# Performance work log

Measured on AMD Instinct MI355X. Metric: run time of the kernel, lower is better.

## Reference

```python
import jax, jax.numpy as jnp
import numpy as np

B, D = 32, 512
N_IMG, N_KN = 50000, 8192
C = 32          # num_classes
R = 16          # image_retrieval_number
K = 8           # knowledge_retrieval_number
NEG = -1e9


def setup_inputs() -> dict:
    key = jax.random.key(0)
    k1, k2, k3, k4, k5 = jax.random.split(key, 5)
    return {
        'query_embeddings': jax.random.normal(k1, (B, D), dtype=jnp.float32),
        'all_image_embeddings': jax.random.normal(k2, (N_IMG, D), dtype=jnp.float32),
        'all_knowledge_embeddings': jax.random.normal(k3, (N_KN, D), dtype=jnp.float32),
        'image_labels': jax.random.randint(k4, (N_IMG,), 0, C, dtype=jnp.int32),
        'knowledge_labels': jax.random.randint(k5, (N_KN,), 0, C, dtype=jnp.int32),
    }


def reference(query_embeddings, all_image_embeddings, all_knowledge_embeddings,
              image_labels, knowledge_labels):
    classes = jnp.arange(C, dtype=jnp.int32)
    img_class_mask = image_labels[None, :] == classes[:, None]       # [C, N_img]
    kn_class_mask = knowledge_labels[None, :] == classes[:, None]    # [C, N_kn]

    # per-class masked similarity retrieval of images
    sims = query_embeddings @ all_image_embeddings.T                 # [B, N_img]
    masked = jnp.where(img_class_mask[None], sims[:, None, :], NEG)  # [B, C, N_img]
    img_vals, img_idx = jax.lax.top_k(masked, R)                     # [B, C, R]
    img_w = jax.nn.softmax(img_vals, axis=-1)
    similar_images = all_image_embeddings[img_idx]                   # [B, C, R, D]

    # image fusion (average of query and attention-weighted retrieved context)
    fused_img = jnp.einsum('bcr,bcrd->bcd', img_w, similar_images)
    enhanced_images = 0.5 * (query_embeddings[:, None, :] + fused_img)  # [B, C, D]

    # class-masked knowledge retrieval for every retrieved image
    ksims = jnp.einsum('bcrd,nd->bcrn', similar_images, all_knowledge_embeddings)
    kmasked = jnp.where(kn_class_mask[None, :, None, :], ksims, NEG)  # [B, C, R, N_kn]
    k_vals, k_idx = jax.lax.top_k(kmasked, K)                         # [B, C, R, K]
    k_w = jax.nn.softmax(k_vals, axis=-1)
    selected_knowledge = all_knowledge_embeddings[k_idx]              # [B, C, R, K, D]

    # knowledge fusion: weight over K, then over R with image weights, average w/ query
    fused_k = jnp.einsum('bcrk,bcrkd->bcrd', k_w, selected_knowledge)
    fused_k = jnp.einsum('bcr,bcrd->bcd', img_w, fused_k)
    enhanced_knowledge = 0.5 * (query_embeddings[:, None, :] + fused_k)  # [B, C, D]

    return enhanced_images, enhanced_knowledge
```

## Files before the change

### kernel.cpp

```cpp
#include <hip/hip_runtime.h>
#include <math.h>

#define NIMG 50000
#define NKN  8192
#define BB   32
#define DD   512
#define CC   32
#define RR   16
#define KK   8
#define MMAX 384
#define NC   7

typedef float f4v __attribute__((ext_vector_type(4)));

__global__ __launch_bounds__(256) void build_lists(const int* __restrict__ labels,
                                                   int n, int* __restrict__ cnt,
                                                   int* __restrict__ list, int stride) {
    int i = blockIdx.x * 256 + threadIdx.x;
    if (i < n) {
        int c = labels[i];
        int pos = atomicAdd(&cnt[c], 1);
        list[c * stride + pos] = i;
    }
}

__global__ __launch_bounds__(64) void sims_kernel(const float* __restrict__ Q,
                                                  const float* __restrict__ I,
                                                  float* __restrict__ S) {
    int n = blockIdx.x * 64 + threadIdx.x;
    if (n >= NIMG) return;
    float acc[BB];
#pragma unroll
    for (int b = 0; b < BB; b++) acc[b] = 0.f;
    const float4* row = (const float4*)(I + (size_t)n * DD);
    const float4* q4 = (const float4*)Q;
    for (int d4 = 0; d4 < DD / 4; d4++) {
        float4 v = row[d4];
#pragma unroll
        for (int b = 0; b < BB; b++) {
            float4 q = q4[b * (DD / 4) + d4];
            acc[b] += v.x * q.x + v.y * q.y + v.z * q.z + v.w * q.w;
        }
    }
#pragma unroll
    for (int b = 0; b < BB; b++) S[(size_t)b * NIMG + n] = acc[b];
}

__global__ __launch_bounds__(256) void topk_img(const float* __restrict__ S,
                                                const int* __restrict__ cnt,
                                                const int* __restrict__ list,
                                                int* __restrict__ t_idx,
                                                float* __restrict__ t_w) {
    int c = blockIdx.x, b = blockIdx.y, tid = threadIdx.x;
    int wave = tid >> 6, lane = tid & 63;
    __shared__ float wv_s[4];
    __shared__ int   wi_s[4];
    __shared__ float kv_s[RR];
    __shared__ int   ki_s[RR];

    int m = cnt[c];
    const float* Sb = S + (size_t)b * NIMG;

    float cv0, cv1, cv2, cv3, cv4, cv5, cv6;
    int   ci0, ci1, ci2, ci3, ci4, ci5, ci6;
#define LOADC(t) { int j = tid + t * 256; \
        if (j < m) { int n = list[c * NIMG + j]; cv##t = Sb[n]; ci##t = n; } \
        else { cv##t = -1e30f; ci##t = 0x7fffffff; } }
    LOADC(0) LOADC(1) LOADC(2) LOADC(3) LOADC(4) LOADC(5) LOADC(6)
#undef LOADC

    unsigned used = 0;
#define CANDT(t) { if (!(used & (1u << t)) && \
                       (cv##t > mv || (cv##t == mv && ci##t < mj))) \
                   { mv = cv##t; mj = ci##t; mt = t; } }
#define RND(k) { \
        float mv = -1e30f; int mj = 0x7fffffff; int mt = -1; \
        CANDT(0) CANDT(1) CANDT(2) CANDT(3) CANDT(4) CANDT(5) CANDT(6) \
        int lmj = mj; \
        for (int off = 32; off > 0; off >>= 1) { \
            float ov = __shfl_xor(mv, off); \
            int   oj = __shfl_xor(mj, off); \
            if (ov > mv || (ov == mv && oj < mj)) { mv = ov; mj = oj; } \
        } \
        if (lane == 0) { wv_s[wave] = mv; wi_s[wave] = mj; } \
        __syncthreads(); \
        float gv = wv_s[0]; int gj = wi_s[0]; \
        if (wv_s[1] > gv || (wv_s[1] == gv && wi_s[1] < gj)) { gv = wv_s[1]; gj = wi_s[1]; } \
        if (wv_s[2] > gv || (wv_s[2] == gv && wi_s[2] < gj)) { gv = wv_s[2]; gj = wi_s[2]; } \
        if (wv_s[3] > gv || (wv_s[3] == gv && wi_s[3] < gj)) { gv = wv_s[3]; gj = wi_s[3]; } \
        if (mt >= 0 && lmj == gj && lmj != 0x7fffffff) used |= (1u << mt); \
        if (tid == 0) { kv_s[k] = gv; ki_s[k] = gj; } \
        __syncthreads(); }

    RND(0)  RND(1)  RND(2)  RND(3)  RND(4)  RND(5)  RND(6)  RND(7)
    RND(8)  RND(9)  RND(10) RND(11) RND(12) RND(13) RND(14) RND(15)
#undef RND
#undef CANDT

    if (tid == 0) {
        float mx = kv_s[0], s = 0.f, e[RR];
#pragma unroll
        for (int k = 0; k < RR; k++) { e[k] = expf(kv_s[k] - mx); s += e[k]; }
        float inv = 1.f / s;
        size_t o = ((size_t)(b * CC) + c) * RR;
#pragma unroll
        for (int k = 0; k < RR; k++) { t_w[o + k] = e[k] * inv; t_idx[o + k] = ki_s[k]; }
    }
}

__global__ __launch_bounds__(256) void img_kernel(const float* __restrict__ Q,
                                                  const float* __restrict__ I,
                                                  const int* __restrict__ t_idx,
                                                  const float* __restrict__ t_w,
                                                  float* __restrict__ out) {
    int c = blockIdx.x, b = blockIdx.y, tid = threadIdx.x;
    __shared__ float w[RR];
    __shared__ int   id[RR];
    if (tid < RR) {
        size_t o = ((size_t)(b * CC) + c) * RR;
        w[tid] = t_w[o + tid]; id[tid] = t_idx[o + tid];
    }
    __syncthreads();
    for (int d = tid; d < DD; d += 256) {
        float acc = 0.f;
#pragma unroll
        for (int r = 0; r < RR; r++) acc += w[r] * I[(size_t)id[r] * DD + d];
        out[((size_t)(b * CC) + c) * DD + d] = 0.5f * (Q[b * DD + d] + acc);
    }
}

__global__ __launch_bounds__(256) void transpose_kn(const float* __restrict__ KN,
                                                    const int* __restrict__ kcnt,
                                                    const int* __restrict__ klist,
                                                    float4* __restrict__ KT4) {
    int c = blockIdx.x;
    int w = threadIdx.x >> 6, lane = threadIdx.x & 63;
    int j = blockIdx.y * 4 + w;
    int m = kcnt[c]; if (m > MMAX) m = MMAX;
    int row = klist[c * NKN + (j < m ? j : 0)];
    const float4* src = (const float4*)(KN + (size_t)row * DD);
    float4* dst = KT4 + (size_t)c * (DD / 4) * MMAX;
    float4 v0 = src[lane], v1 = src[lane + 64];
    dst[(size_t)lane * MMAX + j]        = v0;
    dst[(size_t)(lane + 64) * MMAX + j] = v1;
}

__global__ __launch_bounds__(256, 4) void knowledge_kernel(const float* __restrict__ Q,
                                                           const float* __restrict__ I,
                                                           const float* __restrict__ KN,
                                                           const float4* __restrict__ KT4,
                                                           const int* __restrict__ kcnt,
                                                           const int* __restrict__ klist,
                                                           const int* __restrict__ t_idx,
                                                           const float* __restrict__ t_w,
                                                           float* __restrict__ outk) {
    int c = blockIdx.x, b = blockIdx.y;
    int tid = threadIdx.x, wave = tid >> 6, lane = tid & 63;
    int rbase = wave * 4;

    __shared__ float4 simg[RR][DD / 4];
    __shared__ float  s_iw[RR];
    __shared__ int    s_ii[RR];
    __shared__ float  wgt[RR][KK];
    __shared__ int    kidx[RR][KK];

    if (tid < RR) {
        size_t o = ((size_t)(b * CC) + c) * RR;
        s_iw[tid] = t_w[o + tid]; s_ii[tid] = t_idx[o + tid];
    }
    __syncthreads();

    for (int i = tid; i < RR * DD / 4; i += 256) {
        int r = i >> 7, d4 = i & 127;
        simg[r][d4] = ((const float4*)(I + (size_t)s_ii[r] * DD))[d4];
    }

    int m = kcnt[c]; if (m > MMAX) m = MMAX;
    int ng = (m + 63) >> 6;
    const float4* KTc = KT4 + (size_t)c * (DD / 4) * MMAX;

    f4v A0 = 0.f, A1 = 0.f, A2 = 0.f, A3 = 0.f, A4 = 0.f, A5 = 0.f;

    __syncthreads();

#define LG(g) float4 kk##g = p[g * 64];
#define FG(g, rr) A##g[rr] = fmaf(kk##g.x, u.x, fmaf(kk##g.y, u.y, \
                   fmaf(kk##g.z, u.z, fmaf(kk##g.w, u.w, A##g[rr]))));
#define RRBLK(rr, FMAS) { float4 u = simg[rbase + rr][d4]; FMAS }
#define SCORE(LOADS, F0, F1, F2, F3) \
        for (int d4 = 0; d4 < DD / 4; d4++) { \
            const float4* p = KTc + (size_t)d4 * MMAX + lane; \
            LOADS \
            RRBLK(0, F0) RRBLK(1, F1) RRBLK(2, F2) RRBLK(3, F3) }

    if (ng <= 4) {
        SCORE(LG(0) LG(1) LG(2) LG(3),
              FG(0,0) FG(1,0) FG(2,0) FG(3,0),
              FG(0,1) FG(1,1) FG(2,1) FG(3,1),
              FG(0,2) FG(1,2) FG(2,2) FG(3,2),
              FG(0,3) FG(1,3) FG(2,3) FG(3,3))
    } else if (ng == 5) {
        SCORE(LG(0) LG(1) LG(2) LG(3) LG(4),
              FG(0,0) FG(1,0) FG(2,0) FG(3,0) FG(4,0),
              FG(0,1) FG(1,1) FG(2,1) FG(3,1) FG(4,1),
              FG(0,2) FG(1,2) FG(2,2) FG(3,2) FG(4,2),
              FG(0,3) FG(1,3) FG(2,3) FG(3,3) FG(4,3))
    } else {
        SCORE(LG(0) LG(1) LG(2) LG(3) LG(4) LG(5),
              FG(0,0) FG(1,0) FG(2,0) FG(3,0) FG(4,0) FG(5,0),
              FG(0,1) FG(1,1) FG(2,1) FG(3,1) FG(4,1) FG(5,1),
              FG(0,2) FG(1,2) FG(2,2) FG(3,2) FG(4,2) FG(5,2),
              FG(0,3) FG(1,3) FG(2,3) FG(3,3) FG(4,3) FG(5,3))
    }
#undef SCORE
#undef RRBLK
#undef FG
#undef LG

#define CAND(t) { if (!(used & (1u << t)) && \
                      (lv##t > mv || (lv##t == mv && (t * 64 + lane) < mj))) \
                  { mv = lv##t; mj = t * 64 + lane; mt = t; } }

#define ROUND(k) { \
        float mv = -1e30f; int mj = 0x7fffffff; int mt = -1; \
        CAND(0) CAND(1) CAND(2) CAND(3) CAND(4) CAND(5) \
        int cj = mj; \
        for (int off = 32; off > 0; off >>= 1) { \
            float ov = __shfl_xor(mv, off); \
            int   oj = __shfl_xor(mj, off); \
            if (ov > mv || (ov == mv && oj < mj)) { mv = ov; mj = oj; } \
        } \
        if (cj == mj && mt >= 0) used |= (1u << mt); \
        if (lane == k) myj = mj; \
        kv##k = mv; }

#define TOPK_RR(rr) { \
        int r = rbase + rr; \
        float lv0 = (0 * 64 + lane < m) ? A0[rr] : -1e30f; \
        float lv1 = (1 * 64 + lane < m) ? A1[rr] : -1e30f; \
        float lv2 = (2 * 64 + lane < m) ? A2[rr] : -1e30f; \
        float lv3 = (3 * 64 + lane < m) ? A3[rr] : -1e30f; \
        float lv4 = (4 * 64 + lane < m) ? A4[rr] : -1e30f; \
        float lv5 = (5 * 64 + lane < m) ? A5[rr] : -1e30f; \
        unsigned used = 0; int myj = 0; \
        float kv0, kv1, kv2, kv3, kv4, kv5, kv6, kv7; \
        ROUND(0) ROUND(1) ROUND(2) ROUND(3) \
        ROUND(4) ROUND(5) ROUND(6) ROUND(7) \
        if (lane < KK) kidx[r][lane] = klist[c * NKN + myj]; \
        if (lane == 0) { \
            float e0 = 1.f; \
            float e1 = expf(kv1 - kv0), e2 = expf(kv2 - kv0), e3 = expf(kv3 - kv0); \
            float e4 = expf(kv4 - kv0), e5 = expf(kv5 - kv0), e6 = expf(kv6 - kv0); \
            float e7 = expf(kv7 - kv0); \
            float s = e0 + e1 + e2 + e3 + e4 + e5 + e6 + e7; \
            float wr = s_iw[r] / s; \
            wgt[r][0] = e0 * wr; wgt[r][1] = e1 * wr; wgt[r][2] = e2 * wr; \
            wgt[r][3] = e3 * wr; wgt[r][4] = e4 * wr; wgt[r][5] = e5 * wr; \
            wgt[r][6] = e6 * wr; wgt[r][7] = e7 * wr; \
        } }

    TOPK_RR(0) TOPK_RR(1) TOPK_RR(2) TOPK_RR(3)
#undef TOPK_RR
#undef ROUND
#undef CAND

    __syncthreads();

    float acc0 = 0.f, acc1 = 0.f;
#pragma unroll 8
    for (int p = 0; p < RR * KK; p++) {
        int r = p >> 3, k = p & 7;
        float w = wgt[r][k];
        const float* kp = KN + (size_t)kidx[r][k] * DD;
        acc0 += w * kp[tid];
        acc1 += w * kp[tid + 256];
    }
    size_t o = ((size_t)(b * CC) + c) * DD;
    outk[o + tid]       = 0.5f * (Q[b * DD + tid] + acc0);
    outk[o + tid + 256] = 0.5f * (Q[b * DD + tid + 256] + acc1);
}

extern "C" void kernel_launch(void* const* d_in, const int* in_sizes, int n_in,
                              void* d_out, int out_size, void* d_ws, size_t ws_size,
                              hipStream_t stream) {
    const float* Q  = (const float*)d_in[0];
    const float* I  = (const float*)d_in[1];
    const float* KN = (const float*)d_in[2];
    const int* ilab = (const int*)d_in[3];
    const int* klab = (const int*)d_in[4];

    char* ws = (char*)d_ws;
    float* S        = (float*)ws;  ws += (size_t)BB * NIMG * 4;
    int*   img_list = (int*)ws;    ws += (size_t)CC * NIMG * 4;
    int*   kn_list  = (int*)ws;    ws += (size_t)CC * NKN * 4;
    int*   t_idx    = (int*)ws;    ws += (size_t)BB * CC * RR * 4;
    float* t_w      = (float*)ws;  ws += (size_t)BB * CC * RR * 4;
    int*   img_cnt  = (int*)ws;    ws += CC * 4;
    int*   kn_cnt   = (int*)ws;    ws += CC * 4;
    ws = (char*)(((size_t)ws + 255) & ~(size_t)255);
    float4* KT4     = (float4*)ws; ws += (size_t)CC * (DD / 4) * MMAX * 16;

    float* out_img = (float*)d_out;
    float* out_kn  = out_img + (size_t)BB * CC * DD;

    hipMemsetAsync(img_cnt, 0, 2 * CC * 4, stream);

    build_lists<<<(NIMG + 255) / 256, 256, 0, stream>>>(ilab, NIMG, img_cnt, img_list, NIMG);
    build_lists<<<(NKN  + 255) / 256, 256, 0, stream>>>(klab, NKN,  kn_cnt,  kn_list,  NKN);
    transpose_kn<<<dim3(CC, MMAX / 4), 256, 0, stream>>>(KN, kn_cnt, kn_list, KT4);
    sims_kernel<<<(NIMG + 63) / 64, 64, 0, stream>>>(Q, I, S);
    topk_img<<<dim3(CC, BB), 256, 0, stream>>>(S, img_cnt, img_list, t_idx, t_w);
    img_kernel<<<dim3(CC, BB), 256, 0, stream>>>(Q, I, t_idx, t_w, (float*)d_out);
    knowledge_kernel<<<dim3(CC, BB), 256, 0, stream>>>(Q, I, KN, KT4, kn_cnt, kn_list, t_idx, t_w, out_kn);
}
```

Baseline: 439.4 us.

## Split-K the query-image similarity kernel with LDS-staged queries and two rows per thread

The similarity kernel now splits the 512-wide dot product into four slices across a second grid dimension. Each block stages its query slice in shared memory, and each thread computes two image rows, so every query load is reused twice. A new combine kernel sums the four partial similarity buffers. The goal is more parallelism, since the old version launched only 782 small blocks, and less redundant query traffic. The cost is four times the workspace for partial sums plus an extra read/write pass over them.

```diff
diff --git a/kernel.cpp b/kernel.cpp
--- a/kernel.cpp
+++ b/kernel.cpp
@@ -9,7 +9,8 @@
 #define RR   16
 #define KK   8
 #define MMAX 384
-#define NC   7
+#define SPLIT 4
+#define SD4  (DD / 4 / SPLIT)
 
 typedef float f4v __attribute__((ext_vector_type(4)));
 
@@ -24,26 +25,56 @@
     }
 }
 
-__global__ __launch_bounds__(64) void sims_kernel(const float* __restrict__ Q,
-                                                  const float* __restrict__ I,
-                                                  float* __restrict__ S) {
-    int n = blockIdx.x * 64 + threadIdx.x;
-    if (n >= NIMG) return;
-    float acc[BB];
-#pragma unroll
-    for (int b = 0; b < BB; b++) acc[b] = 0.f;
-    const float4* row = (const float4*)(I + (size_t)n * DD);
-    const float4* q4 = (const float4*)Q;
-    for (int d4 = 0; d4 < DD / 4; d4++) {
-        float4 v = row[d4];
+__global__ __launch_bounds__(256, 2) void sims_kernel(const float* __restrict__ Q,
+                                                      const float* __restrict__ I,
+                                                      float* __restrict__ SP) {
+    int slice = blockIdx.y, tid = threadIdx.x;
+    __shared__ float4 qs[BB][SD4];
+    for (int i = tid; i < BB * SD4; i += 256) {
+        int b = i / SD4, d = i % SD4;
+        qs[b][d] = ((const float4*)Q)[b * (DD / 4) + slice * SD4 + d];
+    }
+    __syncthreads();
+
+    int n0 = blockIdx.x * 512 + tid;
+    int n1 = n0 + 256;
+    bool v1ok = n1 < NIMG;
+    int n1c = v1ok ? n1 : 0;
+
+    float a0[BB], a1[BB];
+#pragma unroll
+    for (int b = 0; b < BB; b++) { a0[b] = 0.f; a1[b] = 0.f; }
+
+    const float4* r0 = (const float4*)(I + (size_t)n0 * DD) + slice * SD4;
+    const float4* r1 = (const float4*)(I + (size_t)n1c * DD) + slice * SD4;
+    for (int d = 0; d < SD4; d++) {
+        float4 x0 = r0[d], x1 = r1[d];
 #pragma unroll
         for (int b = 0; b < BB; b++) {
-            float4 q = q4[b * (DD / 4) + d4];
-            acc[b] += v.x * q.x + v.y * q.y + v.z * q.z + v.w * q.w;
+            float4 q = qs[b][d];
+            a0[b] += x0.x * q.x + x0.y * q.y + x0.z * q.z + x0.w * q.w;
+            a1[b] += x1.x * q.x + x1.y * q.y + x1.z * q.z + x1.w * q.w;
         }
     }
-#pragma unroll
-    for (int b = 0; b < BB; b++) S[(size_t)b * NIMG + n] = acc[b];
+    float* out = SP + (size_t)slice * BB * NIMG;
+#pragma unroll
+    for (int b = 0; b < BB; b++) {
+        out[(size_t)b * NIMG + n0] = a0[b];
+        if (v1ok) out[(size_t)b * NIMG + n1] = a1[b];
+    }
+}
+
+__global__ __launch_bounds__(256) void combine_s(float4* __restrict__ SP) {
+    int i = blockIdx.x * 256 + threadIdx.x;
+    const int n4 = BB * NIMG / 4;
+    if (i >= n4) return;
+    float4 s0 = SP[i], s1 = SP[i + n4], s2 = SP[i + 2 * n4], s3 = SP[i + 3 * n4];
+    float4 r;
+    r.x = ((s0.x + s1.x) + s2.x) + s3.x;
+    r.y = ((s0.y + s1.y) + s2.y) + s3.y;
+    r.z = ((s0.z + s1.z) + s2.z) + s3.z;
+    r.w = ((s0.w + s1.w) + s2.w) + s3.w;
+    SP[i] = r;
 }
 
 __global__ __launch_bounds__(256) void topk_img(const float* __restrict__ S,
@@ -290,7 +321,7 @@
     const int* klab = (const int*)d_in[4];
 
     char* ws = (char*)d_ws;
-    float* S        = (float*)ws;  ws += (size_t)BB * NIMG * 4;
+    float* SP       = (float*)ws;  ws += (size_t)SPLIT * BB * NIMG * 4;
     int*   img_list = (int*)ws;    ws += (size_t)CC * NIMG * 4;
     int*   kn_list  = (int*)ws;    ws += (size_t)CC * NKN * 4;
     int*   t_idx    = (int*)ws;    ws += (size_t)BB * CC * RR * 4;
@@ -308,8 +339,9 @@
     build_lists<<<(NIMG + 255) / 256, 256, 0, stream>>>(ilab, NIMG, img_cnt, img_list, NIMG);
     build_lists<<<(NKN  + 255) / 256, 256, 0, stream>>>(klab, NKN,  kn_cnt,  kn_list,  NKN);
     transpose_kn<<<dim3(CC, MMAX / 4), 256, 0, stream>>>(KN, kn_cnt, kn_list, KT4);
-    sims_kernel<<<(NIMG + 63) / 64, 64, 0, stream>>>(Q, I, S);
-    topk_img<<<dim3(CC, BB), 256, 0, stream>>>(S, img_cnt, img_list, t_idx, t_w);
+    sims_kernel<<<dim3((NIMG + 511) / 512, SPLIT), 256, 0, stream>>>(Q, I, SP);
+    combine_s<<<(BB * NIMG / 4 + 255) / 256, 256, 0, stream>>>((float4*)SP);
+    topk_img<<<dim3(CC, BB), 256, 0, stream>>>(SP, img_cnt, img_list, t_idx, t_w);
     img_kernel<<<dim3(CC, BB), 256, 0, stream>>>(Q, I, t_idx, t_w, (float*)d_out);
     knowledge_kernel<<<dim3(CC, BB), 256, 0, stream>>>(Q, I, KN, KT4, kn_cnt, kn_list, t_idx, t_w, out_kn);
 }
```

Measured after the change: 366.6 us. -16.6%, faster.
